# Optimization experiments

Hardware: AMD Instinct MI355X
Metric: run time of the kernel (lower is better)

Reference implementation:

```python
import jax, jax.numpy as jnp
import numpy as np
import math

D_MODEL = 1024
NUM_HEADS = 16
D_KV = 64
INNER = NUM_HEADS * D_KV
NUM_BUCKETS = 32
MAX_DISTANCE = 128


def _relative_position_bucket(relative_position, num_buckets=NUM_BUCKETS, max_distance=MAX_DISTANCE):
    # bidirectional T5 bucketing
    n = -relative_position
    num_buckets = num_buckets // 2
    ret = (n < 0).astype(jnp.int32) * num_buckets
    n = jnp.abs(n)
    max_exact = num_buckets // 2
    is_small = n < max_exact
    n_safe = jnp.maximum(n, 1).astype(jnp.float32)  # avoid log(0); masked by is_small
    val_if_large = max_exact + (
        jnp.log(n_safe / max_exact) / math.log(max_distance / max_exact) * (num_buckets - max_exact)
    ).astype(jnp.int32)
    val_if_large = jnp.minimum(val_if_large, num_buckets - 1)
    return jnp.where(is_small, n, val_if_large) + ret


def _position_bias(rel_emb, q_len, k_len):
    ctx = jnp.arange(q_len)[:, None]
    mem = jnp.arange(k_len)[None, :]
    buckets = _relative_position_bucket(mem - ctx)          # [q, k]
    values = rel_emb[buckets]                               # [q, k, H]
    return jnp.transpose(values, (2, 0, 1))[None]           # [1, H, q, k]


def setup_inputs() -> dict:
    key = jax.random.key(0)
    ks = jax.random.split(key, 6)
    B, S = 2, 2048
    scale = 1.0 / math.sqrt(D_MODEL)
    return {
        "hidden_states": jax.random.normal(ks[0], (B, S, D_MODEL), dtype=jnp.float32),
        "mask": jnp.zeros((B, 1, 1, S), dtype=jnp.float32),
        "Wq": jax.random.normal(ks[1], (D_MODEL, INNER), dtype=jnp.float32) * scale,
        "Wk": jax.random.normal(ks[2], (D_MODEL, INNER), dtype=jnp.float32) * scale,
        "Wv": jax.random.normal(ks[3], (D_MODEL, INNER), dtype=jnp.float32) * scale,
        "Wo": jax.random.normal(ks[4], (INNER, D_MODEL), dtype=jnp.float32) * scale,
        "rel_emb": jax.random.normal(ks[5], (NUM_BUCKETS, NUM_HEADS), dtype=jnp.float32),
    }


def reference(hidden_states, mask, Wq, Wk, Wv, Wo, rel_emb):
    B, S, _ = hidden_states.shape
    def split_heads(x):
        return jnp.transpose(x.reshape(B, -1, NUM_HEADS, D_KV), (0, 2, 1, 3))  # [B,H,S,d]
    q = split_heads(hidden_states @ Wq)
    k = split_heads(hidden_states @ Wk)
    v = split_heads(hidden_states @ Wv)
    scores = jnp.einsum("bhqd,bhkd->bhqk", q, k)            # unscaled, T5-style
    position_bias = _position_bias(rel_emb, S, S)           # [1,H,S,S]
    scores = scores + position_bias + mask
    attn = jax.nn.softmax(scores, axis=-1)
    context = jnp.einsum("bhqk,bhkd->bhqd", attn, v)
    context = jnp.transpose(context, (0, 2, 1, 3)).reshape(B, S, INNER)
    output = context @ Wo
    return output, position_bias
```

## Files before the change

### kernel.cpp

```cpp
#include <hip/hip_runtime.h>
#include <cstdint>

#define AS1 __attribute__((address_space(1)))
#define AS3 __attribute__((address_space(3)))

typedef _Float16 half8 __attribute__((ext_vector_type(8)));
typedef _Float16 half4_t __attribute__((ext_vector_type(4)));
typedef float v4f __attribute__((ext_vector_type(4)));

__device__ __forceinline__ void async_ld16(const void* g, void* l) {
  __builtin_amdgcn_global_load_lds((const AS1 uint32_t*)g, (AS3 uint32_t*)l, 16, 0, 0);
}

__device__ __forceinline__ int t5_bucket(int delta) {
  int n = -delta;
  int ret = 0;
  if (n < 0) { ret = 16; n = -n; }
  if (n < 8) return n + ret;
  if (n >= 91) return 15 + ret;
  if ((n & (n - 1)) == 0) {
    int l = 31 - __clz(n);
    int v = 2 + 2 * l;
    return (v > 15 ? 15 : v) + ret;
  }
  int v = 8 + (int)(logf((float)n * 0.125f) * (8.0f / logf(16.0f)));
  return (v > 15 ? 15 : v) + ret;
}

__global__ void k_prep(const float* __restrict__ hs, const float* __restrict__ Wq,
                       const float* __restrict__ Wk, const float* __restrict__ Wv,
                       const float* __restrict__ Wo, _Float16* __restrict__ hsF,
                       _Float16* __restrict__ wqkvT, _Float16* __restrict__ woT) {
  const int tid = threadIdx.x;
  if (blockIdx.x < 4096) {
    int t = blockIdx.x * 256 + tid;
    float4 f = ((const float4*)hs)[t];
    half4_t h = {(_Float16)f.x, (_Float16)f.y, (_Float16)f.z, (_Float16)f.w};
    ((half4_t*)hsF)[t] = h;
    return;
  }
  __shared__ float tile[32][33];
  const int idx = blockIdx.x - 4096;
  const int z = idx >> 10, rem = idx & 1023;
  const float* src = (z == 0) ? Wq : (z == 1) ? Wk : (z == 2) ? Wv : Wo;
  _Float16* dst = (z < 3) ? (wqkvT + ((size_t)z << 20)) : woT;
  const int tx = tid & 31, ty = tid >> 5;
  const int bx = (rem & 31) * 32, by = (rem >> 5) * 32;
#pragma unroll
  for (int i = 0; i < 32; i += 8)
    tile[ty + i][tx] = src[(size_t)(by + ty + i) * 1024 + bx + tx];
  __syncthreads();
#pragma unroll
  for (int i = 0; i < 32; i += 8)
    dst[(size_t)(bx + ty + i) * 1024 + by + tx] = (_Float16)tile[tx][ty + i];
}

__global__ __launch_bounds__(256, 3) void k_gemm_qkv_bias(
    const _Float16* __restrict__ A, const _Float16* __restrict__ BT,
    _Float16* __restrict__ qkv, _Float16* __restrict__ vT,
    const float* __restrict__ rel, float* __restrict__ outb) {
  __shared__ __align__(16) _Float16 As[128 * 32];
  __shared__ __align__(16) _Float16 Bs[128 * 32];
  __shared__ float btab[256];
  const int tid = threadIdx.x;
  const int wave = tid >> 6, lane = tid & 63;
  const int l15 = lane & 15, quad = lane >> 4;
  const int m0 = blockIdx.y * 128, n0 = blockIdx.x * 128;
  const int wm = (wave >> 1) * 64, wn = (wave & 1) * 64;
  const int r0 = tid >> 2, c0 = (tid & 3) * 8;
  constexpr int K = 1024;

  const int bid = blockIdx.y * 24 + blockIdx.x;
  const bool do_bias = bid < 512;
  const int hB = bid >> 5;
  const int qoff = (bid & 31) * 64;
  float c_past = 0.f, c_fut = 0.f;
  if (do_bias) {
    btab[tid & 255] = rel[t5_bucket((tid & 255) - 128) * 16 + hB];
    c_past = rel[15 * 16 + hB];
    c_fut = rel[31 * 16 + hB];
  }

  v4f acc[4][4] = {};
  for (int k0 = 0; k0 < K; k0 += 32) {
    asm volatile("s_waitcnt lgkmcnt(0)\ns_barrier" ::: "memory");
    async_ld16(A + (size_t)(m0 + r0) * K + k0 + c0, (char*)As + (size_t)(wave * 64) * 16);
    async_ld16(A + (size_t)(m0 + 64 + r0) * K + k0 + c0,
               (char*)As + (size_t)(256 + wave * 64) * 16);
    async_ld16(BT + (size_t)(n0 + r0) * K + k0 + c0, (char*)Bs + (size_t)(wave * 64) * 16);
    async_ld16(BT + (size_t)(n0 + 64 + r0) * K + k0 + c0,
               (char*)Bs + (size_t)(256 + wave * 64) * 16);

    if (do_bias) {
      __builtin_amdgcn_sched_barrier(0);
      const int iter = k0 >> 5;
#pragma unroll
      for (int j = 0; j < 2; ++j) {
        int fi = iter * 512 + j * 256 + tid;
        int qr = qoff + (fi >> 8);
        int c = fi & 255;
        int k4 = ((c >> 4) << 5) + (c & 15);
        int kb = k4 << 2;
        float4 v;
        if (kb - qr >= 91) {
          v = make_float4(c_fut, c_fut, c_fut, c_fut);
        } else if (qr - kb - 3 >= 91) {
          v = make_float4(c_past, c_past, c_past, c_past);
        } else {
          v.x = btab[kb + 0 - qr + 128];
          v.y = btab[kb + 1 - qr + 128];
          v.z = btab[kb + 2 - qr + 128];
          v.w = btab[kb + 3 - qr + 128];
        }
        ((float4*)outb)[((size_t)hB * 2048 + qr) * 512 + k4] = v;
      }
      asm volatile("s_waitcnt vmcnt(2) lgkmcnt(0)\ns_barrier" ::: "memory");
    } else {
      asm volatile("s_waitcnt vmcnt(0) lgkmcnt(0)\ns_barrier" ::: "memory");
    }

    half8 af[4], bf[4];
#pragma unroll
    for (int mt = 0; mt < 4; ++mt)
      af[mt] = *(const half8*)(As + (wm + mt * 16 + l15) * 32 + quad * 8);
#pragma unroll
    for (int nt = 0; nt < 4; ++nt)
      bf[nt] = *(const half8*)(Bs + (wn + nt * 16 + l15) * 32 + quad * 8);
#pragma unroll
    for (int mt = 0; mt < 4; ++mt)
#pragma unroll
      for (int nt = 0; nt < 4; ++nt)
        acc[mt][nt] = __builtin_amdgcn_mfma_f32_16x16x32_f16(af[mt], bf[nt], acc[mt][nt], 0, 0, 0);
  }
  if (n0 >= 2048) {
#pragma unroll
    for (int mt = 0; mt < 4; ++mt)
#pragma unroll
      for (int nt = 0; nt < 4; ++nt) {
        int col = n0 + wn + nt * 16 + l15 - 2048;
        int row0 = m0 + wm + mt * 16 + quad * 4;
        int bb = row0 >> 11, s0 = row0 & 2047;
        half4_t hv = {(_Float16)acc[mt][nt][0], (_Float16)acc[mt][nt][1],
                      (_Float16)acc[mt][nt][2], (_Float16)acc[mt][nt][3]};
        *(half4_t*)(vT + ((size_t)bb * 1024 + col) * 2048 + s0) = hv;
      }
    return;
  }
#pragma unroll
  for (int mt = 0; mt < 4; ++mt)
#pragma unroll
    for (int nt = 0; nt < 4; ++nt)
#pragma unroll
      for (int r = 0; r < 4; ++r)
        qkv[(size_t)(m0 + wm + mt * 16 + quad * 4 + r) * 3072 + n0 + wn + nt * 16 + l15] =
            (_Float16)acc[mt][nt][r];
}

__global__ __launch_bounds__(256, 2) void k_gemm_n64(const _Float16* __restrict__ A,
                                                     const _Float16* __restrict__ BT,
                                                     float* __restrict__ C, int K, int ldc) {
  __shared__ __align__(16) _Float16 As[128 * 32];
  __shared__ __align__(16) _Float16 Bs[64 * 32];
  const int tid = threadIdx.x;
  const int wave = tid >> 6, lane = tid & 63;
  const int l15 = lane & 15, quad = lane >> 4;
  const int m0 = blockIdx.y * 128, n0 = blockIdx.x * 64;
  const int wm = (wave >> 1) * 64, wn = (wave & 1) * 32;
  const int r0 = tid >> 2, c0 = (tid & 3) * 8;
  v4f acc[4][2] = {};
  for (int k0 = 0; k0 < K; k0 += 32) {
    asm volatile("s_waitcnt lgkmcnt(0)\ns_barrier" ::: "memory");
    async_ld16(A + (size_t)(m0 + r0) * K + k0 + c0, (char*)As + (size_t)(wave * 64) * 16);
    async_ld16(A + (size_t)(m0 + 64 + r0) * K + k0 + c0,
               (char*)As + (size_t)(256 + wave * 64) * 16);
    async_ld16(BT + (size_t)(n0 + r0) * K + k0 + c0, (char*)Bs + (size_t)(wave * 64) * 16);
    asm volatile("s_waitcnt vmcnt(0) lgkmcnt(0)\ns_barrier" ::: "memory");
    half8 af[4], bf[2];
#pragma unroll
    for (int mt = 0; mt < 4; ++mt)
      af[mt] = *(const half8*)(As + (wm + mt * 16 + l15) * 32 + quad * 8);
#pragma unroll
    for (int nt = 0; nt < 2; ++nt)
      bf[nt] = *(const half8*)(Bs + (wn + nt * 16 + l15) * 32 + quad * 8);
#pragma unroll
    for (int mt = 0; mt < 4; ++mt)
#pragma unroll
      for (int nt = 0; nt < 2; ++nt)
        acc[mt][nt] = __builtin_amdgcn_mfma_f32_16x16x32_f16(af[mt], bf[nt], acc[mt][nt], 0, 0, 0);
  }
#pragma unroll
  for (int mt = 0; mt < 4; ++mt)
#pragma unroll
    for (int nt = 0; nt < 2; ++nt)
#pragma unroll
      for (int r = 0; r < 4; ++r)
        C[(size_t)(m0 + wm + mt * 16 + quad * 4 + r) * ldc + n0 + wn + nt * 16 + l15] =
            acc[mt][nt][r];
}

__global__ __launch_bounds__(256, 2) void k_attn(const _Float16* __restrict__ qkv,
                                                 const _Float16* __restrict__ vT,
                                                 const float* __restrict__ mask,
                                                 const float* __restrict__ rel,
                                                 _Float16* __restrict__ ctx,
                                                 float* __restrict__ outb) {
  constexpr int S = 2048, LD = 3072;
  __shared__ __align__(16) _Float16 Ks[2][64 * 72];
  __shared__ __align__(16) _Float16 VT[2][64 * 72];
  __shared__ __align__(16) _Float16 Psh[128 * 72];
  __shared__ float btab[512];
  const int tid = threadIdx.x, wave = tid >> 6, lane = tid & 63;
  const int l15 = lane & 15, quad = lane >> 4;
  const int flat = blockIdx.x + 16 * (blockIdx.y + 16 * blockIdx.z);
  const int swz = (flat & 7) * 64 + (flat >> 3);
  const int q0 = (swz & 15) * 128, h = (swz >> 4) & 15, b = swz >> 8;

  for (int j = tid; j < 512; j += 256) btab[j] = rel[t5_bucket(j - 256) * 16 + h];
  const float c_past = rel[15 * 16 + h];
  const float c_fut = rel[31 * 16 + h];

  half8 bq[2][2];
#pragma unroll
  for (int qt = 0; qt < 2; ++qt) {
    const _Float16* qp = qkv + (size_t)(b * S + q0 + wave * 32 + qt * 16 + l15) * LD + h * 64;
    bq[qt][0] = *(const half8*)(qp + quad * 8);
    bq[qt][1] = *(const half8*)(qp + 32 + quad * 8);
  }
  v4f o[2][4] = {};
  float mrun[2] = {-INFINITY, -INFINITY};
  float lrun[2] = {0.f, 0.f};

  const int srow = tid >> 2, scol = (tid & 3) * 8;
  const _Float16* kg = qkv + (size_t)(b * S + srow) * LD + 1024 + h * 64 + scol;
  const _Float16* vg = vT + ((size_t)((b * 16 + h) * 64 + srow)) * S + scol;
  const float4* mkp = (const float4*)(mask + (size_t)b * S);

  const int qrow0 = q0 + b * 64;
  float4* const bias_base = (float4*)outb + ((size_t)h * 2048 + qrow0) * 512;

  {
    half8 kr0 = *(const half8*)(kg);
    half8 kr1 = *(const half8*)(kg + 32);
    half8 vr0 = *(const half8*)(vg);
    half8 vr1 = *(const half8*)(vg + 32);
    *(half8*)(&Ks[0][srow * 72 + scol]) = kr0;
    *(half8*)(&Ks[0][srow * 72 + scol + 32]) = kr1;
    *(half8*)(&VT[0][srow * 72 + scol]) = vr0;
    *(half8*)(&VT[0][srow * 72 + scol + 32]) = vr1;
  }
  float4 mk[4];
#pragma unroll
  for (int mt = 0; mt < 4; ++mt) mk[mt] = mkp[mt * 4 + quad];
  __syncthreads();

  for (int kv0 = 0; kv0 < S; kv0 += 64) {
    const int buf = (kv0 >> 6) & 1;
    const bool more = (kv0 + 64) < S;
    half8 kr0n, kr1n, vr0n, vr1n;
    float4 mkn[4];
    if (more) {
      kr0n = *(const half8*)(kg + (size_t)(kv0 + 64) * LD);
      kr1n = *(const half8*)(kg + (size_t)(kv0 + 64) * LD + 32);
      vr0n = *(const half8*)(vg + kv0 + 64);
      vr1n = *(const half8*)(vg + kv0 + 64 + 32);
#pragma unroll
      for (int mt = 0; mt < 4; ++mt) mkn[mt] = mkp[((kv0 + 64) >> 2) + mt * 4 + quad];
    }

    if (kv0 & 64) {
      const int diffw = kv0 - qrow0;
      float4* dst = bias_base + (kv0 >> 2);
      if (diffw >= 154) {
        const float4 v = make_float4(c_fut, c_fut, c_fut, c_fut);
#pragma unroll
        for (int j = 0; j < 4; ++j) {
          int fi = j * 256 + tid;
          dst[(size_t)(fi >> 4) * 512 + (fi & 15)] = v;
        }
      } else if (diffw <= -154) {
        const float4 v = make_float4(c_past, c_past, c_past, c_past);
#pragma unroll
        for (int j = 0; j < 4; ++j) {
          int fi = j * 256 + tid;
          dst[(size_t)(fi >> 4) * 512 + (fi & 15)] = v;
        }
      } else {
#pragma unroll
        for (int j = 0; j < 4; ++j) {
          int fi = j * 256 + tid;
          int row = fi >> 4, c4 = fi & 15;
          int q = qrow0 + row, k = kv0 + c4 * 4;
          float4 v;
          if (k - q >= 91) {
            v = make_float4(c_fut, c_fut, c_fut, c_fut);
          } else if (q - k - 3 >= 91) {
            v = make_float4(c_past, c_past, c_past, c_past);
          } else {
            int bi = k - q + 256;
            v.x = btab[bi + 0];
            v.y = btab[bi + 1];
            v.z = btab[bi + 2];
            v.w = btab[bi + 3];
          }
          dst[(size_t)row * 512 + c4] = v;
        }
      }
    }

    const _Float16* KsB = &Ks[buf][0];
    const _Float16* VTB = &VT[buf][0];
    v4f sc[2][4] = {};
    __builtin_amdgcn_s_setprio(1);
#pragma unroll
    for (int kc = 0; kc < 2; ++kc)
#pragma unroll
      for (int mt = 0; mt < 4; ++mt) {
        half8 af = *(const half8*)(KsB + (mt * 16 + l15) * 72 + kc * 32 + quad * 8);
        sc[0][mt] = __builtin_amdgcn_mfma_f32_16x16x32_f16(af, bq[0][kc], sc[0][mt], 0, 0, 0);
        sc[1][mt] = __builtin_amdgcn_mfma_f32_16x16x32_f16(af, bq[1][kc], sc[1][mt], 0, 0, 0);
      }
    __builtin_amdgcn_s_setprio(0);

    const int diff = kv0 - q0;
    const bool mixed = (diff >= -153) && (diff <= 217);
    const float cf = (diff >= 218) ? c_fut : c_past;
    v4f cm[4];
#pragma unroll
    for (int mt = 0; mt < 4; ++mt) {
      cm[mt][0] = mk[mt].x; cm[mt][1] = mk[mt].y; cm[mt][2] = mk[mt].z; cm[mt][3] = mk[mt].w;
      if (!mixed) {
        cm[mt][0] += cf; cm[mt][1] += cf; cm[mt][2] += cf; cm[mt][3] += cf;
      }
    }
    if (mixed) {
#pragma unroll
      for (int qt = 0; qt < 2; ++qt) {
        const int qq = q0 + wave * 32 + qt * 16 + l15;
#pragma unroll
        for (int mt = 0; mt < 4; ++mt) {
          int base = kv0 + mt * 16 + quad * 4 - qq + 256;
#pragma unroll
          for (int r = 0; r < 4; ++r) sc[qt][mt][r] += btab[base + r] + cm[mt][r];
        }
      }
    } else {
#pragma unroll
      for (int qt = 0; qt < 2; ++qt)
#pragma unroll
        for (int mt = 0; mt < 4; ++mt)
#pragma unroll
          for (int r = 0; r < 4; ++r) sc[qt][mt][r] += cm[mt][r];
    }

#pragma unroll
    for (int qt = 0; qt < 2; ++qt) {
      v4f m4 = sc[qt][0];
#pragma unroll
      for (int r = 0; r < 4; ++r) {
        m4[r] = fmaxf(m4[r], sc[qt][1][r]);
        m4[r] = fmaxf(m4[r], sc[qt][2][r]);
        m4[r] = fmaxf(m4[r], sc[qt][3][r]);
      }
      float mx = fmaxf(fmaxf(m4[0], m4[1]), fmaxf(m4[2], m4[3]));
      mx = fmaxf(mx, __shfl_xor(mx, 16, 64));
      mx = fmaxf(mx, __shfl_xor(mx, 32, 64));
      if (!__all(mx <= mrun[qt])) {
        float mnew = fmaxf(mrun[qt], mx);
        float alpha = __expf(mrun[qt] - mnew);
        mrun[qt] = mnew;
        lrun[qt] *= alpha;
#pragma unroll
        for (int dt = 0; dt < 4; ++dt)
#pragma unroll
          for (int r = 0; r < 4; ++r) o[qt][dt][r] *= alpha;
      }
      const float mcur = mrun[qt];
      v4f s4 = {};
#pragma unroll
      for (int mt = 0; mt < 4; ++mt)
#pragma unroll
        for (int r = 0; r < 4; ++r) {
          float p = __expf(sc[qt][mt][r] - mcur);
          sc[qt][mt][r] = p;
          s4[r] += p;
        }
      float rs = (s4[0] + s4[1]) + (s4[2] + s4[3]);
      rs += __shfl_xor(rs, 16, 64);
      rs += __shfl_xor(rs, 32, 64);
      lrun[qt] += rs;
      const int prow = wave * 32 + qt * 16 + l15;
#pragma unroll
      for (int mt = 0; mt < 4; ++mt) {
        half4_t ph = {(_Float16)sc[qt][mt][0], (_Float16)sc[qt][mt][1],
                      (_Float16)sc[qt][mt][2], (_Float16)sc[qt][mt][3]};
        *(half4_t*)(Psh + prow * 72 + mt * 16 + quad * 4) = ph;
      }
    }

    __builtin_amdgcn_s_setprio(1);
#pragma unroll
    for (int kc = 0; kc < 2; ++kc) {
      half8 bp0 = *(const half8*)(Psh + (wave * 32 + l15) * 72 + kc * 32 + quad * 8);
      half8 bp1 = *(const half8*)(Psh + (wave * 32 + 16 + l15) * 72 + kc * 32 + quad * 8);
#pragma unroll
      for (int dt = 0; dt < 4; ++dt) {
        half8 av = *(const half8*)(VTB + (dt * 16 + l15) * 72 + kc * 32 + quad * 8);
        o[0][dt] = __builtin_amdgcn_mfma_f32_16x16x32_f16(av, bp0, o[0][dt], 0, 0, 0);
        o[1][dt] = __builtin_amdgcn_mfma_f32_16x16x32_f16(av, bp1, o[1][dt], 0, 0, 0);
      }
    }
    __builtin_amdgcn_s_setprio(0);

    if (more) {
      _Float16* Kn = &Ks[buf ^ 1][0];
      _Float16* Vn = &VT[buf ^ 1][0];
      *(half8*)(Kn + srow * 72 + scol) = kr0n;
      *(half8*)(Kn + srow * 72 + scol + 32) = kr1n;
      *(half8*)(Vn + srow * 72 + scol) = vr0n;
      *(half8*)(Vn + srow * 72 + scol + 32) = vr1n;
      asm volatile("s_waitcnt lgkmcnt(0)\ns_barrier" ::: "memory");
#pragma unroll
      for (int mt = 0; mt < 4; ++mt) mk[mt] = mkn[mt];
    }
  }
#pragma unroll
  for (int qt = 0; qt < 2; ++qt) {
    float inv = 1.0f / lrun[qt];
    const size_t token = (size_t)(b * S + q0 + wave * 32 + qt * 16 + l15);
#pragma unroll
    for (int dt = 0; dt < 4; ++dt) {
      half4_t hv = {(_Float16)(o[qt][dt][0] * inv), (_Float16)(o[qt][dt][1] * inv),
                    (_Float16)(o[qt][dt][2] * inv), (_Float16)(o[qt][dt][3] * inv)};
      *(half4_t*)(ctx + token * 1024 + h * 64 + dt * 16 + quad * 4) = hv;
    }
  }
}

extern "C" void kernel_launch(void* const* d_in, const int* in_sizes, int n_in,
                              void* d_out, int out_size, void* d_ws, size_t ws_size,
                              hipStream_t stream) {
  const float* hs = (const float*)d_in[0];
  const float* mask = (const float*)d_in[1];
  const float* Wq = (const float*)d_in[2];
  const float* Wk = (const float*)d_in[3];
  const float* Wv = (const float*)d_in[4];
  const float* Wo = (const float*)d_in[5];
  const float* rel = (const float*)d_in[6];
  float* out = (float*)d_out;

  char* ws = (char*)d_ws;
  _Float16* hsF = (_Float16*)(ws);
  _Float16* wqkvT = (_Float16*)(ws + (8u << 20));
  _Float16* woT = (_Float16*)(ws + (14u << 20));
  _Float16* qkv = (_Float16*)(ws + (16u << 20));
  _Float16* ctx = (_Float16*)(ws + (40u << 20));
  _Float16* vT = (_Float16*)(ws + (48u << 20));

  k_prep<<<8192, 256, 0, stream>>>(hs, Wq, Wk, Wv, Wo, hsF, wqkvT, woT);

  k_gemm_qkv_bias<<<dim3(24, 32), 256, 0, stream>>>(hsF, wqkvT, qkv, vT, rel,
                                                    out + 4194304);
  k_attn<<<dim3(16, 16, 2), 256, 0, stream>>>(qkv, vT, mask, rel, ctx, out + 4194304);
  k_gemm_n64<<<dim3(16, 32), 256, 0, stream>>>(ctx, woT, out, 1024, 1024);
}
```

Measured before the change: 421.1 us.

## Split attention block across eight waves with one 16-row query tile each

The attention kernel now launches 512 threads per block, so each of eight waves handles 16 query rows instead of four waves handling 32 rows each. Per-thread register state (scores, output accumulators, softmax stats) halves and the K/V staging and bias writes are spread over more threads. The aim is more waves in flight for latency hiding. The cost is that every K/V fragment read from LDS is reused by fewer MFMAs, there are more waves meeting at each barrier, and occupancy now also depends on the launch-bounds hint of 4 blocks.

```diff
diff --git a/kernel.cpp b/kernel.cpp
--- a/kernel.cpp
+++ b/kernel.cpp
@@ -198,7 +198,7 @@
             acc[mt][nt][r];
 }
 
-__global__ __launch_bounds__(256, 2) void k_attn(const _Float16* __restrict__ qkv,
+__global__ __launch_bounds__(512, 4) void k_attn(const _Float16* __restrict__ qkv,
                                                  const _Float16* __restrict__ vT,
                                                  const float* __restrict__ mask,
                                                  const float* __restrict__ rel,
@@ -215,22 +215,21 @@
   const int swz = (flat & 7) * 64 + (flat >> 3);
   const int q0 = (swz & 15) * 128, h = (swz >> 4) & 15, b = swz >> 8;
 
-  for (int j = tid; j < 512; j += 256) btab[j] = rel[t5_bucket(j - 256) * 16 + h];
+  btab[tid] = rel[t5_bucket((int)tid - 256) * 16 + h];
   const float c_past = rel[15 * 16 + h];
   const float c_fut = rel[31 * 16 + h];
 
-  half8 bq[2][2];
-#pragma unroll
-  for (int qt = 0; qt < 2; ++qt) {
-    const _Float16* qp = qkv + (size_t)(b * S + q0 + wave * 32 + qt * 16 + l15) * LD + h * 64;
-    bq[qt][0] = *(const half8*)(qp + quad * 8);
-    bq[qt][1] = *(const half8*)(qp + 32 + quad * 8);
-  }
-  v4f o[2][4] = {};
-  float mrun[2] = {-INFINITY, -INFINITY};
-  float lrun[2] = {0.f, 0.f};
-
-  const int srow = tid >> 2, scol = (tid & 3) * 8;
+  half8 bq[2];
+  {
+    const _Float16* qp = qkv + (size_t)(b * S + q0 + wave * 16 + l15) * LD + h * 64;
+    bq[0] = *(const half8*)(qp + quad * 8);
+    bq[1] = *(const half8*)(qp + 32 + quad * 8);
+  }
+  v4f o[4] = {};
+  float mrun = -INFINITY;
+  float lrun = 0.f;
+
+  const int srow = tid >> 3, scol = (tid & 7) * 8;
   const _Float16* kg = qkv + (size_t)(b * S + srow) * LD + 1024 + h * 64 + scol;
   const _Float16* vg = vT + ((size_t)((b * 16 + h) * 64 + srow)) * S + scol;
   const float4* mkp = (const float4*)(mask + (size_t)b * S);
@@ -239,14 +238,10 @@
   float4* const bias_base = (float4*)outb + ((size_t)h * 2048 + qrow0) * 512;
 
   {
-    half8 kr0 = *(const half8*)(kg);
-    half8 kr1 = *(const half8*)(kg + 32);
-    half8 vr0 = *(const half8*)(vg);
-    half8 vr1 = *(const half8*)(vg + 32);
-    *(half8*)(&Ks[0][srow * 72 + scol]) = kr0;
-    *(half8*)(&Ks[0][srow * 72 + scol + 32]) = kr1;
-    *(half8*)(&VT[0][srow * 72 + scol]) = vr0;
-    *(half8*)(&VT[0][srow * 72 + scol + 32]) = vr1;
+    half8 kr = *(const half8*)(kg);
+    half8 vr = *(const half8*)(vg);
+    *(half8*)(&Ks[0][srow * 72 + scol]) = kr;
+    *(half8*)(&VT[0][srow * 72 + scol]) = vr;
   }
   float4 mk[4];
 #pragma unroll
@@ -256,13 +251,11 @@
   for (int kv0 = 0; kv0 < S; kv0 += 64) {
     const int buf = (kv0 >> 6) & 1;
     const bool more = (kv0 + 64) < S;
-    half8 kr0n, kr1n, vr0n, vr1n;
+    half8 krn, vrn;
     float4 mkn[4];
     if (more) {
-      kr0n = *(const half8*)(kg + (size_t)(kv0 + 64) * LD);
-      kr1n = *(const half8*)(kg + (size_t)(kv0 + 64) * LD + 32);
-      vr0n = *(const half8*)(vg + kv0 + 64);
-      vr1n = *(const half8*)(vg + kv0 + 64 + 32);
+      krn = *(const half8*)(kg + (size_t)(kv0 + 64) * LD);
+      vrn = *(const half8*)(vg + kv0 + 64);
 #pragma unroll
       for (int mt = 0; mt < 4; ++mt) mkn[mt] = mkp[((kv0 + 64) >> 2) + mt * 4 + quad];
     }
@@ -273,21 +266,21 @@
       if (diffw >= 154) {
         const float4 v = make_float4(c_fut, c_fut, c_fut, c_fut);
 #pragma unroll
-        for (int j = 0; j < 4; ++j) {
-          int fi = j * 256 + tid;
+        for (int j = 0; j < 2; ++j) {
+          int fi = j * 512 + tid;
           dst[(size_t)(fi >> 4) * 512 + (fi & 15)] = v;
         }
       } else if (diffw <= -154) {
         const float4 v = make_float4(c_past, c_past, c_past, c_past);
 #pragma unroll
-        for (int j = 0; j < 4; ++j) {
-          int fi = j * 256 + tid;
+        for (int j = 0; j < 2; ++j) {
+          int fi = j * 512 + tid;
           dst[(size_t)(fi >> 4) * 512 + (fi & 15)] = v;
         }
       } else {
 #pragma unroll
-        for (int j = 0; j < 4; ++j) {
-          int fi = j * 256 + tid;
+        for (int j = 0; j < 2; ++j) {
+          int fi = j * 512 + tid;
           int row = fi >> 4, c4 = fi & 15;
           int q = qrow0 + row, k = kv0 + c4 * 4;
           float4 v;
@@ -309,15 +302,14 @@
 
     const _Float16* KsB = &Ks[buf][0];
     const _Float16* VTB = &VT[buf][0];
-    v4f sc[2][4] = {};
+    v4f sc[4] = {};
     __builtin_amdgcn_s_setprio(1);
 #pragma unroll
     for (int kc = 0; kc < 2; ++kc)
 #pragma unroll
       for (int mt = 0; mt < 4; ++mt) {
         half8 af = *(const half8*)(KsB + (mt * 16 + l15) * 72 + kc * 32 + quad * 8);
-        sc[0][mt] = __builtin_amdgcn_mfma_f32_16x16x32_f16(af, bq[0][kc], sc[0][mt], 0, 0, 0);
-        sc[1][mt] = __builtin_amdgcn_mfma_f32_16x16x32_f16(af, bq[1][kc], sc[1][mt], 0, 0, 0);
+        sc[mt] = __builtin_amdgcn_mfma_f32_16x16x32_f16(af, bq[kc], sc[mt], 0, 0, 0);
       }
     __builtin_amdgcn_s_setprio(0);
 
@@ -333,66 +325,60 @@
       }
     }
     if (mixed) {
-#pragma unroll
-      for (int qt = 0; qt < 2; ++qt) {
-        const int qq = q0 + wave * 32 + qt * 16 + l15;
-#pragma unroll
-        for (int mt = 0; mt < 4; ++mt) {
-          int base = kv0 + mt * 16 + quad * 4 - qq + 256;
-#pragma unroll
-          for (int r = 0; r < 4; ++r) sc[qt][mt][r] += btab[base + r] + cm[mt][r];
-        }
+      const int qq = q0 + wave * 16 + l15;
+#pragma unroll
+      for (int mt = 0; mt < 4; ++mt) {
+        int base = kv0 + mt * 16 + quad * 4 - qq + 256;
+#pragma unroll
+        for (int r = 0; r < 4; ++r) sc[mt][r] += btab[base + r] + cm[mt][r];
       }
     } else {
 #pragma unroll
-      for (int qt = 0; qt < 2; ++qt)
-#pragma unroll
-        for (int mt = 0; mt < 4; ++mt)
-#pragma unroll
-          for (int r = 0; r < 4; ++r) sc[qt][mt][r] += cm[mt][r];
-    }
-
-#pragma unroll
-    for (int qt = 0; qt < 2; ++qt) {
-      v4f m4 = sc[qt][0];
+      for (int mt = 0; mt < 4; ++mt)
+#pragma unroll
+        for (int r = 0; r < 4; ++r) sc[mt][r] += cm[mt][r];
+    }
+
+    {
+      v4f m4 = sc[0];
 #pragma unroll
       for (int r = 0; r < 4; ++r) {
-        m4[r] = fmaxf(m4[r], sc[qt][1][r]);
-        m4[r] = fmaxf(m4[r], sc[qt][2][r]);
-        m4[r] = fmaxf(m4[r], sc[qt][3][r]);
+        m4[r] = fmaxf(m4[r], sc[1][r]);
+        m4[r] = fmaxf(m4[r], sc[2][r]);
+        m4[r] = fmaxf(m4[r], sc[3][r]);
       }
       float mx = fmaxf(fmaxf(m4[0], m4[1]), fmaxf(m4[2], m4[3]));
       mx = fmaxf(mx, __shfl_xor(mx, 16, 64));
       mx = fmaxf(mx, __shfl_xor(mx, 32, 64));
-      if (!__all(mx <= mrun[qt])) {
-        float mnew = fmaxf(mrun[qt], mx);
-        float alpha = __expf(mrun[qt] - mnew);
-        mrun[qt] = mnew;
-        lrun[qt] *= alpha;
+      if (!__all(mx <= mrun)) {
+        float mnew = fmaxf(mrun, mx);
+        float alpha = __expf(mrun - mnew);
+        mrun = mnew;
+        lrun *= alpha;
 #pragma unroll
         for (int dt = 0; dt < 4; ++dt)
 #pragma unroll
-          for (int r = 0; r < 4; ++r) o[qt][dt][r] *= alpha;
-      }
-      const float mcur = mrun[qt];
+          for (int r = 0; r < 4; ++r) o[dt][r] *= alpha;
+      }
+      const float mcur = mrun;
       v4f s4 = {};
 #pragma unroll
       for (int mt = 0; mt < 4; ++mt)
 #pragma unroll
         for (int r = 0; r < 4; ++r) {
-          float p = __expf(sc[qt][mt][r] - mcur);
-          sc[qt][mt][r] = p;
+          float p = __expf(sc[mt][r] - mcur);
+          sc[mt][r] = p;
           s4[r] += p;
         }
       float rs = (s4[0] + s4[1]) + (s4[2] + s4[3]);
       rs += __shfl_xor(rs, 16, 64);
       rs += __shfl_xor(rs, 32, 64);
-      lrun[qt] += rs;
-      const int prow = wave * 32 + qt * 16 + l15;
+      lrun += rs;
+      const int prow = wave * 16 + l15;
 #pragma unroll
       for (int mt = 0; mt < 4; ++mt) {
-        half4_t ph = {(_Float16)sc[qt][mt][0], (_Float16)sc[qt][mt][1],
-                      (_Float16)sc[qt][mt][2], (_Float16)sc[qt][mt][3]};
+        half4_t ph = {(_Float16)sc[mt][0], (_Float16)sc[mt][1],
+                      (_Float16)sc[mt][2], (_Float16)sc[mt][3]};
         *(half4_t*)(Psh + prow * 72 + mt * 16 + quad * 4) = ph;
       }
     }
@@ -400,13 +386,11 @@
     __builtin_amdgcn_s_setprio(1);
 #pragma unroll
     for (int kc = 0; kc < 2; ++kc) {
-      half8 bp0 = *(const half8*)(Psh + (wave * 32 + l15) * 72 + kc * 32 + quad * 8);
-      half8 bp1 = *(const half8*)(Psh + (wave * 32 + 16 + l15) * 72 + kc * 32 + quad * 8);
+      half8 bp = *(const half8*)(Psh + (wave * 16 + l15) * 72 + kc * 32 + quad * 8);
 #pragma unroll
       for (int dt = 0; dt < 4; ++dt) {
         half8 av = *(const half8*)(VTB + (dt * 16 + l15) * 72 + kc * 32 + quad * 8);
-        o[0][dt] = __builtin_amdgcn_mfma_f32_16x16x32_f16(av, bp0, o[0][dt], 0, 0, 0);
-        o[1][dt] = __builtin_amdgcn_mfma_f32_16x16x32_f16(av, bp1, o[1][dt], 0, 0, 0);
+        o[dt] = __builtin_amdgcn_mfma_f32_16x16x32_f16(av, bp, o[dt], 0, 0, 0);
       }
     }
     __builtin_amdgcn_s_setprio(0);
@@ -414,23 +398,20 @@
     if (more) {
       _Float16* Kn = &Ks[buf ^ 1][0];
       _Float16* Vn = &VT[buf ^ 1][0];
-      *(half8*)(Kn + srow * 72 + scol) = kr0n;
-      *(half8*)(Kn + srow * 72 + scol + 32) = kr1n;
-      *(half8*)(Vn + srow * 72 + scol) = vr0n;
-      *(half8*)(Vn + srow * 72 + scol + 32) = vr1n;
+      *(half8*)(Kn + srow * 72 + scol) = krn;
+      *(half8*)(Vn + srow * 72 + scol) = vrn;
       asm volatile("s_waitcnt lgkmcnt(0)\ns_barrier" ::: "memory");
 #pragma unroll
       for (int mt = 0; mt < 4; ++mt) mk[mt] = mkn[mt];
     }
   }
-#pragma unroll
-  for (int qt = 0; qt < 2; ++qt) {
-    float inv = 1.0f / lrun[qt];
-    const size_t token = (size_t)(b * S + q0 + wave * 32 + qt * 16 + l15);
+  {
+    float inv = 1.0f / lrun;
+    const size_t token = (size_t)(b * S + q0 + wave * 16 + l15);
 #pragma unroll
     for (int dt = 0; dt < 4; ++dt) {
-      half4_t hv = {(_Float16)(o[qt][dt][0] * inv), (_Float16)(o[qt][dt][1] * inv),
-                    (_Float16)(o[qt][dt][2] * inv), (_Float16)(o[qt][dt][3] * inv)};
+      half4_t hv = {(_Float16)(o[dt][0] * inv), (_Float16)(o[dt][1] * inv),
+                    (_Float16)(o[dt][2] * inv), (_Float16)(o[dt][3] * inv)};
       *(half4_t*)(ctx + token * 1024 + h * 64 + dt * 16 + quad * 4) = hv;
     }
   }
@@ -460,6 +441,6 @@
 
   k_gemm_qkv_bias<<<dim3(24, 32), 256, 0, stream>>>(hsF, wqkvT, qkv, vT, rel,
                                                     out + 4194304);
-  k_attn<<<dim3(16, 16, 2), 256, 0, stream>>>(qkv, vT, mask, rel, ctx, out + 4194304);
+  k_attn<<<dim3(16, 16, 2), 512, 0, stream>>>(qkv, vT, mask, rel, ctx, out + 4194304);
   k_gemm_n64<<<dim3(16, 32), 256, 0, stream>>>(ctx, woT, out, 1024, 1024);
 }
```

Result: no change. 420.7 us (-0.1%).
